# Optimization experiments

Measured on AMD Instinct MI355X. Metric: run time of the kernel, lower is better.

## Reference

```python
import jax, jax.numpy as jnp
import numpy as np

BATCH, DIM, HEADS = 512, 2048, 16
CPH = DIM // HEADS  # per-head channels = 128
EPS = 1e-5


def setup_inputs() -> dict:
    key = jax.random.key(0)
    ks = jax.random.split(key, 6)
    x = jax.random.normal(ks[0], (BATCH, DIM, 1, 1), dtype=jnp.float32)
    W_qv = jax.random.normal(ks[1], (2 * DIM, DIM), dtype=jnp.float32) * (1.0 / np.sqrt(DIM))
    temperature = jnp.ones((HEADS, 1, 1), dtype=jnp.float32)
    k_param = jax.random.normal(ks[2], (BATCH, DIM, 1, 1), dtype=jnp.float32)
    bias_param = jax.random.normal(ks[3], (BATCH, HEADS, CPH * CPH, 1), dtype=jnp.float32)
    bn_gamma = jnp.ones((HEADS,), dtype=jnp.float32)
    bn_beta = jnp.zeros((HEADS,), dtype=jnp.float32)
    W_out = jax.random.normal(ks[4], (DIM, DIM, 1, 1), dtype=jnp.float32) * (1.0 / np.sqrt(DIM))
    b_out = jax.random.normal(ks[5], (DIM,), dtype=jnp.float32) * 0.01
    return {"x": x, "W_qv": W_qv, "temperature": temperature, "k_param": k_param,
            "bias_param": bias_param, "bn_gamma": bn_gamma, "bn_beta": bn_beta,
            "W_out": W_out, "b_out": b_out}


def reference(x, W_qv, temperature, k_param, bias_param, bn_gamma, bn_beta, W_out, b_out):
    b, c, h, w = x.shape  # h = w = 1 (required by x.squeeze() + Linear)
    heads = temperature.shape[0]
    cph = c // heads

    xs = x.reshape(b, c)
    qv = xs @ W_qv.T                     # [b, 2c]
    q, v = qv[:, :c], qv[:, c:]
    q = q.reshape(b, heads, cph, 1)      # b head c (h w)
    v = v.reshape(b, heads, cph, 1)
    k = k_param.reshape(b, heads, cph, 1)

    # BatchNorm2d over channel = head (training-mode batch stats, biased var)
    mean = jnp.mean(v, axis=(0, 2, 3), keepdims=True)
    var = jnp.var(v, axis=(0, 2, 3), keepdims=True)
    v = (v - mean) * jax.lax.rsqrt(var + EPS)
    v = v * bn_gamma.reshape(1, heads, 1, 1) + bn_beta.reshape(1, heads, 1, 1)

    # attn = q @ k^T over the singleton spatial dim -> [b, head, cph, cph]
    attn = jnp.einsum('bhcx,bhdx->bhcd', q, k)
    attn = attn + bias_param.reshape(b, heads, cph, cph)
    attn = attn * temperature  # [heads,1,1] broadcasts over batch
    attn = jax.nn.softmax(attn, axis=-1)

    out = jnp.einsum('bhcd,bhdx->bhcx', attn, v)  # [b, head, cph, 1]
    out = out.reshape(b, c)

    # 1x1 conv == matmul
    out = out @ W_out.reshape(c, c).T + b_out
    return out.reshape(b, c, 1, 1)
```

## Files before the change

### kernel.cpp

```cpp
#include <hip/hip_runtime.h>
#include <hip/hip_bf16.h>
#include <cstdint>

#define NBATCH 512
#define NDIM   2048
#define NHEADS 16
#define NCPH   128

typedef __bf16 bf16x8 __attribute__((ext_vector_type(8)));
typedef __bf16 bf16x4 __attribute__((ext_vector_type(4)));
typedef float  f32x4  __attribute__((ext_vector_type(4)));

__device__ __forceinline__ unsigned short f2bf(float f) {
    uint32_t u = __builtin_bit_cast(uint32_t, f);
    u += 0x7FFFu + ((u >> 16) & 1u);
    return (unsigned short)(u >> 16);
}

__device__ __forceinline__ void gl_lds16(const void* g, void* l) {
    __builtin_amdgcn_global_load_lds(
        (const __attribute__((address_space(1))) void*)g,
        (__attribute__((address_space(3))) void*)l,
        16, 0, 0);
}

__global__ __launch_bounds__(256) void cvt_x(
    const float* __restrict__ x, unsigned short* __restrict__ ox)
{
    const int t = blockIdx.x * 256 + threadIdx.x;
    float4 v = ((const float4*)x)[t];
    ushort4 o;
    o.x = f2bf(v.x); o.y = f2bf(v.y); o.z = f2bf(v.z); o.w = f2bf(v.w);
    ((ushort4*)ox)[t] = o;
}

template<int BN, int BK, bool BNP>
__global__ __launch_bounds__(256) void gemm_tall(
    const unsigned short* __restrict__ Abf, const float* __restrict__ Bf,
    float* __restrict__ C, const float* __restrict__ bias,
    float* __restrict__ bnpart, int M, int N, int K)
{
    constexpr int BM = 128;
    constexpr int MI = 2;
    constexpr int NI = BN / 16;
    constexpr int GA = (BM * BK) / 2048;
    constexpr int BPT4 = (BN * BK) / 1024;
    constexpr int CPRB = BK / 8;

    __shared__ unsigned short As[2][BM * BK];
    __shared__ unsigned short Bs[2][BN * BK];

    const int tid  = threadIdx.x;
    const int lane = tid & 63;
    const int wid  = tid >> 6;
    const int m0   = blockIdx.y * BM;
    const int n0   = blockIdx.x * BN;
    const int fr   = lane & 15;
    const int kq   = lane >> 4;

    f32x4 acc[MI][NI] = {};
    float4 rb[BPT4];

    const int brow = (BPT4 == 2) ? tid / CPRB : tid >> 4;
    const int bch  = (BPT4 == 2) ? tid % CPRB : ((tid & 15) >> 1);
    const int bhalf = (BPT4 == 2) ? 0 : (tid & 1);

    auto loadA = [&](int bs, int k0) {
#pragma unroll
        for (int r = 0; r < GA; r++) {
            const int e    = r * 2048 + tid * 8;
            const int row  = e / BK;
            const int chk  = (e % BK) >> 3;
            gl_lds16(Abf + (size_t)(m0 + row) * K + k0
                         + ((chk ^ (row & 7)) << 3), &As[bs][e]);
        }
    };
    auto loadB = [&](int k0) {
        if constexpr (BPT4 == 2) {
            const float4* g = (const float4*)(Bf + (size_t)(n0 + brow) * K
                                              + k0 + bch * 8);
            rb[0] = g[0];
            rb[1] = g[1];
        } else {
            rb[0] = *(const float4*)(Bf + (size_t)(n0 + brow) * K + k0
                                     + bch * 8 + bhalf * 4);
        }
    };
    auto writeB = [&](int bs) {
        const int base = brow * BK + ((bch ^ (brow & 7)) << 3);
        if constexpr (BPT4 == 2) {
            bf16x8 v;
            v[0] = (__bf16)rb[0].x; v[1] = (__bf16)rb[0].y;
            v[2] = (__bf16)rb[0].z; v[3] = (__bf16)rb[0].w;
            v[4] = (__bf16)rb[1].x; v[5] = (__bf16)rb[1].y;
            v[6] = (__bf16)rb[1].z; v[7] = (__bf16)rb[1].w;
            *(bf16x8*)&Bs[bs][base] = v;
        } else {
            bf16x4 v;
            v[0] = (__bf16)rb[0].x; v[1] = (__bf16)rb[0].y;
            v[2] = (__bf16)rb[0].z; v[3] = (__bf16)rb[0].w;
            *(bf16x4*)&Bs[bs][base + bhalf * 4] = v;
        }
    };
    auto compute = [&](int bs) {
#pragma unroll
        for (int kh = 0; kh < BK / 32; kh++) {
            const int kchunk = kh * 4 + kq;
            bf16x8 af[MI], bfv[NI];
#pragma unroll
            for (int i = 0; i < MI; i++) {
                const int row = wid * 32 + i * 16 + fr;
                af[i] = *(const bf16x8*)&As[bs][row * BK
                        + ((kchunk ^ (row & 7)) << 3)];
            }
#pragma unroll
            for (int j = 0; j < NI; j++) {
                const int row = j * 16 + fr;
                bfv[j] = *(const bf16x8*)&Bs[bs][row * BK
                         + ((kchunk ^ (row & 7)) << 3)];
            }
#pragma unroll
            for (int i = 0; i < MI; i++)
#pragma unroll
                for (int j = 0; j < NI; j++)
                    acc[i][j] = __builtin_amdgcn_mfma_f32_16x16x32_bf16(
                        af[i], bfv[j], acc[i][j], 0, 0, 0);
        }
    };

    loadA(0, 0);
    loadB(0);
    writeB(0);
    __syncthreads();

    const int NT = K / BK;
    int cur = 0;
    for (int t = 0; t < NT - 1; t++) {
        loadB((t + 1) * BK);
        loadA(cur ^ 1, (t + 1) * BK);
        compute(cur);
        writeB(cur ^ 1);
        __syncthreads();
        cur ^= 1;
    }
    compute(cur);

    const int row0 = m0 + wid * 32 + (kq << 2);
    const int col0 = n0 + fr;
#pragma unroll
    for (int j = 0; j < NI; j++) {
        const int cc = col0 + j * 16;
        const float badd = bias ? bias[cc] : 0.0f;
#pragma unroll
        for (int i = 0; i < MI; i++)
#pragma unroll
            for (int r = 0; r < 4; r++)
                C[(size_t)(row0 + i * 16 + r) * N + cc] = acc[i][j][r] + badd;
    }

    if (BNP && n0 >= NDIM) {
        float s = 0.f, ss = 0.f;
#pragma unroll
        for (int i = 0; i < MI; i++)
#pragma unroll
            for (int j = 0; j < NI; j++)
#pragma unroll
                for (int r = 0; r < 4; r++) {
                    const float v = acc[i][j][r];
                    s += v;
                    ss = fmaf(v, v, ss);
                }
#pragma unroll
        for (int off = 32; off; off >>= 1) {
            s  += __shfl_down(s, off);
            ss += __shfl_down(ss, off);
        }
        __shared__ float rs[4], rss[4];
        if (lane == 0) { rs[wid] = s; rss[wid] = ss; }
        __syncthreads();
        if (tid == 0)
            ((float2*)bnpart)[((n0 - NDIM) >> 5) * 4 + (m0 >> 7)] =
                make_float2(rs[0] + rs[1] + rs[2] + rs[3],
                            rss[0] + rss[1] + rss[2] + rss[3]);
    }
}

__global__ __launch_bounds__(256) void attn_k(
    const float* __restrict__ qv, const float* __restrict__ kparam,
    const float* __restrict__ bias, const float* __restrict__ temperature,
    const float* __restrict__ bnpart, const float* __restrict__ gamma,
    const float* __restrict__ beta, unsigned short* __restrict__ aout)
{
    const int bh = blockIdx.x;
    const int b  = bh >> 4;
    const int h  = bh & 15;
    const int tid = threadIdx.x;

    __shared__ float ks[NCPH], vsr[NCPH], s2sh[2];
    if (tid < 32)
        ((float4*)ks)[tid] =
            ((const float4*)(kparam + (size_t)b * NDIM + h * NCPH))[tid];
    else if (tid < 64)
        ((float4*)vsr)[tid - 32] =
            ((const float4*)(qv + (size_t)b * (2 * NDIM) + NDIM + h * NCPH))[tid - 32];

    if (tid < 16) {
        float2 p = ((const float2*)bnpart)[h * 16 + tid];
        float s = p.x, ss = p.y;
#pragma unroll
        for (int off = 8; off; off >>= 1) {
            s  += __shfl_xor(s, off);
            ss += __shfl_xor(ss, off);
        }
        if (tid == 0) {
            const float inv = 1.0f / (NBATCH * NCPH);
            float mean = s * inv;
            float var  = ss * inv - mean * mean;
            float sc   = gamma[h] * rsqrtf(var + 1e-5f);
            s2sh[0] = sc;
            s2sh[1] = beta[h] - mean * sc;
        }
    }

    const int c = tid >> 1, half = tid & 1;
    const float qc   = qv[(size_t)b * (2 * NDIM) + h * NCPH + c];
    const float temp = temperature[h];

    const float4* bp = (const float4*)(bias + ((size_t)bh << 14)
                                       + (size_t)c * NCPH + half * 64);
    float4 l4[16];
#pragma unroll
    for (int j = 0; j < 16; j++) l4[j] = bp[j];

    __syncthreads();
    const float sc = s2sh[0], sh = s2sh[1];
    const float4* kk4 = (const float4*)(ks  + half * 64);
    const float4* vv4 = (const float4*)(vsr + half * 64);

    float s0 = 0.f, s1 = 0.f, o0 = 0.f, o1 = 0.f;
#pragma unroll
    for (int j = 0; j < 16; j++) {
        const float4 bb = l4[j];
        const float4 kx = kk4[j];
        const float4 vx = vv4[j];
        float px = __expf(fmaf(qc, kx.x, bb.x) * temp);
        float py = __expf(fmaf(qc, kx.y, bb.y) * temp);
        float pz = __expf(fmaf(qc, kx.z, bb.z) * temp);
        float pw = __expf(fmaf(qc, kx.w, bb.w) * temp);
        s0 += px; s1 += py; s0 += pz; s1 += pw;
        o0 = fmaf(px, vx.x, o0);
        o1 = fmaf(py, vx.y, o1);
        o0 = fmaf(pz, vx.z, o0);
        o1 = fmaf(pw, vx.w, o1);
    }
    float s = s0 + s1, o = o0 + o1;
    s += __shfl_xor(s, 1);
    o += __shfl_xor(o, 1);

    if (half == 0)
        aout[(size_t)b * NDIM + h * NCPH + c] = f2bf(fmaf(sc, o / s, sh));
}

extern "C" void kernel_launch(void* const* d_in, const int* in_sizes, int n_in,
                              void* d_out, int out_size, void* d_ws, size_t ws_size,
                              hipStream_t stream)
{
    const float* x      = (const float*)d_in[0];
    const float* Wqv    = (const float*)d_in[1];
    const float* temp   = (const float*)d_in[2];
    const float* kparam = (const float*)d_in[3];
    const float* bias   = (const float*)d_in[4];
    const float* gamma  = (const float*)d_in[5];
    const float* beta   = (const float*)d_in[6];
    const float* Wout   = (const float*)d_in[7];
    const float* bout   = (const float*)d_in[8];
    float* out = (float*)d_out;

    char* ws = (char*)d_ws;
    float*          qv     = (float*)(ws);
    unsigned short* ao_bf  = (unsigned short*)(ws + 8388608);
    float*          bnpart = (float*)(ws + 10485760);
    unsigned short* x_bf   = (unsigned short*)(ws + 10487808);

    cvt_x<<<1024, 256, 0, stream>>>(x, x_bf);

    gemm_tall<32, 64, true><<<dim3(128, 4), 256, 0, stream>>>(
        x_bf, Wqv, qv, nullptr, bnpart, NBATCH, 2 * NDIM, NDIM);

    attn_k<<<NBATCH * NHEADS, 256, 0, stream>>>(
        qv, kparam, bias, temp, bnpart, gamma, beta, ao_bf);

    gemm_tall<16, 64, false><<<dim3(128, 4), 256, 0, stream>>>(
        ao_bf, Wout, out, bout, nullptr, NBATCH, NDIM, NDIM);
}
```

Baseline: 184.8 us.

## Keep full-K weight slab resident in LDS and stream A from global registers

Replaces the double-buffered K-tiled GEMM with a kernel that converts a 32-column by full-K slab of the fp32 weights to bf16 once into 128KB of LDS. Each of 8 waves then streams its A rows directly from global memory into registers with a 4-deep software prefetch, with no per-tile barriers. The tile shapes and grids change: the QV GEMM uses BM=256 over 128x2 blocks, and the output GEMM uses BM=128 over 64x4 blocks. The BN partial-stat layout is updated to match. This removes the per-K-step syncs and A staging through LDS, but the large LDS footprint limits occupancy to one block per CU and forces a serial weight-load prologue.

```diff
diff --git a/kernel.cpp b/kernel.cpp
--- a/kernel.cpp
+++ b/kernel.cpp
@@ -8,20 +8,12 @@
 #define NCPH   128
 
 typedef __bf16 bf16x8 __attribute__((ext_vector_type(8)));
-typedef __bf16 bf16x4 __attribute__((ext_vector_type(4)));
 typedef float  f32x4  __attribute__((ext_vector_type(4)));
 
 __device__ __forceinline__ unsigned short f2bf(float f) {
     uint32_t u = __builtin_bit_cast(uint32_t, f);
     u += 0x7FFFu + ((u >> 16) & 1u);
     return (unsigned short)(u >> 16);
-}
-
-__device__ __forceinline__ void gl_lds16(const void* g, void* l) {
-    __builtin_amdgcn_global_load_lds(
-        (const __attribute__((address_space(1))) void*)g,
-        (__attribute__((address_space(3))) void*)l,
-        16, 0, 0);
 }
 
 __global__ __launch_bounds__(256) void cvt_x(
@@ -34,121 +26,77 @@
     ((ushort4*)ox)[t] = o;
 }
 
-template<int BN, int BK, bool BNP>
-__global__ __launch_bounds__(256) void gemm_tall(
+template<int BM, bool BNP>
+__global__ __launch_bounds__(512) void gemm_bres(
     const unsigned short* __restrict__ Abf, const float* __restrict__ Bf,
     float* __restrict__ C, const float* __restrict__ bias,
-    float* __restrict__ bnpart, int M, int N, int K)
-{
-    constexpr int BM = 128;
-    constexpr int MI = 2;
-    constexpr int NI = BN / 16;
-    constexpr int GA = (BM * BK) / 2048;
-    constexpr int BPT4 = (BN * BK) / 1024;
-    constexpr int CPRB = BK / 8;
-
-    __shared__ unsigned short As[2][BM * BK];
-    __shared__ unsigned short Bs[2][BN * BK];
+    float* __restrict__ bnpart, int N)
+{
+    constexpr int MI = BM / 128;
+    __shared__ unsigned short Bs[32 * 2048];
 
     const int tid  = threadIdx.x;
     const int lane = tid & 63;
-    const int wid  = tid >> 6;
+    const int wv   = tid >> 6;
     const int m0   = blockIdx.y * BM;
-    const int n0   = blockIdx.x * BN;
+    const int n0   = blockIdx.x * 32;
     const int fr   = lane & 15;
     const int kq   = lane >> 4;
-
-    f32x4 acc[MI][NI] = {};
-    float4 rb[BPT4];
-
-    const int brow = (BPT4 == 2) ? tid / CPRB : tid >> 4;
-    const int bch  = (BPT4 == 2) ? tid % CPRB : ((tid & 15) >> 1);
-    const int bhalf = (BPT4 == 2) ? 0 : (tid & 1);
-
-    auto loadA = [&](int bs, int k0) {
-#pragma unroll
-        for (int r = 0; r < GA; r++) {
-            const int e    = r * 2048 + tid * 8;
-            const int row  = e / BK;
-            const int chk  = (e % BK) >> 3;
-            gl_lds16(Abf + (size_t)(m0 + row) * K + k0
-                         + ((chk ^ (row & 7)) << 3), &As[bs][e]);
-        }
+    const int mw   = m0 + wv * (MI * 16);
+
+    {
+        const int r  = tid >> 4;
+        const int c0 = tid & 15;
+#pragma unroll
+        for (int it = 0; it < 16; it++) {
+            const int kc = c0 + it * 16;
+            const float4* g = (const float4*)(Bf + (size_t)(n0 + r) * 2048
+                                              + kc * 8);
+            float4 v0 = g[0], v1 = g[1];
+            bf16x8 v;
+            v[0] = (__bf16)v0.x; v[1] = (__bf16)v0.y;
+            v[2] = (__bf16)v0.z; v[3] = (__bf16)v0.w;
+            v[4] = (__bf16)v1.x; v[5] = (__bf16)v1.y;
+            v[6] = (__bf16)v1.z; v[7] = (__bf16)v1.w;
+            *(bf16x8*)&Bs[r * 2048 + ((kc ^ (r & 15)) << 3)] = v;
+        }
+    }
+    __syncthreads();
+
+    f32x4 acc[MI][2] = {};
+    bf16x8 a0[MI], a1[MI], a2[MI], a3[MI];
+
+    auto ldA = [&](bf16x8 (&d)[MI], int t) {
+#pragma unroll
+        for (int i = 0; i < MI; i++)
+            d[i] = *(const bf16x8*)(Abf + (size_t)(mw + i * 16 + fr) * 2048
+                                    + t * 32 + kq * 8);
     };
-    auto loadB = [&](int k0) {
-        if constexpr (BPT4 == 2) {
-            const float4* g = (const float4*)(Bf + (size_t)(n0 + brow) * K
-                                              + k0 + bch * 8);
-            rb[0] = g[0];
-            rb[1] = g[1];
-        } else {
-            rb[0] = *(const float4*)(Bf + (size_t)(n0 + brow) * K + k0
-                                     + bch * 8 + bhalf * 4);
+    auto step = [&](bf16x8 (&a)[MI], int t) {
+#pragma unroll
+        for (int j = 0; j < 2; j++) {
+            const int row = j * 16 + fr;
+            bf16x8 b = *(const bf16x8*)&Bs[row * 2048
+                        + (((4 * t + kq) ^ (row & 15)) << 3)];
+#pragma unroll
+            for (int i = 0; i < MI; i++)
+                acc[i][j] = __builtin_amdgcn_mfma_f32_16x16x32_bf16(
+                    a[i], b, acc[i][j], 0, 0, 0);
         }
     };
-    auto writeB = [&](int bs) {
-        const int base = brow * BK + ((bch ^ (brow & 7)) << 3);
-        if constexpr (BPT4 == 2) {
-            bf16x8 v;
-            v[0] = (__bf16)rb[0].x; v[1] = (__bf16)rb[0].y;
-            v[2] = (__bf16)rb[0].z; v[3] = (__bf16)rb[0].w;
-            v[4] = (__bf16)rb[1].x; v[5] = (__bf16)rb[1].y;
-            v[6] = (__bf16)rb[1].z; v[7] = (__bf16)rb[1].w;
-            *(bf16x8*)&Bs[bs][base] = v;
-        } else {
-            bf16x4 v;
-            v[0] = (__bf16)rb[0].x; v[1] = (__bf16)rb[0].y;
-            v[2] = (__bf16)rb[0].z; v[3] = (__bf16)rb[0].w;
-            *(bf16x4*)&Bs[bs][base + bhalf * 4] = v;
-        }
-    };
-    auto compute = [&](int bs) {
-#pragma unroll
-        for (int kh = 0; kh < BK / 32; kh++) {
-            const int kchunk = kh * 4 + kq;
-            bf16x8 af[MI], bfv[NI];
-#pragma unroll
-            for (int i = 0; i < MI; i++) {
-                const int row = wid * 32 + i * 16 + fr;
-                af[i] = *(const bf16x8*)&As[bs][row * BK
-                        + ((kchunk ^ (row & 7)) << 3)];
-            }
-#pragma unroll
-            for (int j = 0; j < NI; j++) {
-                const int row = j * 16 + fr;
-                bfv[j] = *(const bf16x8*)&Bs[bs][row * BK
-                         + ((kchunk ^ (row & 7)) << 3)];
-            }
-#pragma unroll
-            for (int i = 0; i < MI; i++)
-#pragma unroll
-                for (int j = 0; j < NI; j++)
-                    acc[i][j] = __builtin_amdgcn_mfma_f32_16x16x32_bf16(
-                        af[i], bfv[j], acc[i][j], 0, 0, 0);
-        }
-    };
-
-    loadA(0, 0);
-    loadB(0);
-    writeB(0);
-    __syncthreads();
-
-    const int NT = K / BK;
-    int cur = 0;
-    for (int t = 0; t < NT - 1; t++) {
-        loadB((t + 1) * BK);
-        loadA(cur ^ 1, (t + 1) * BK);
-        compute(cur);
-        writeB(cur ^ 1);
-        __syncthreads();
-        cur ^= 1;
-    }
-    compute(cur);
-
-    const int row0 = m0 + wid * 32 + (kq << 2);
+
+    ldA(a0, 0); ldA(a1, 1); ldA(a2, 2); ldA(a3, 3);
+    for (int t = 0; t < 64; t += 4) {
+        step(a0, t);     if (t + 4 < 64) ldA(a0, t + 4);
+        step(a1, t + 1); if (t + 5 < 64) ldA(a1, t + 5);
+        step(a2, t + 2); if (t + 6 < 64) ldA(a2, t + 6);
+        step(a3, t + 3); if (t + 7 < 64) ldA(a3, t + 7);
+    }
+
+    const int row0 = mw + (kq << 2);
     const int col0 = n0 + fr;
 #pragma unroll
-    for (int j = 0; j < NI; j++) {
+    for (int j = 0; j < 2; j++) {
         const int cc = col0 + j * 16;
         const float badd = bias ? bias[cc] : 0.0f;
 #pragma unroll
@@ -163,7 +111,7 @@
 #pragma unroll
         for (int i = 0; i < MI; i++)
 #pragma unroll
-            for (int j = 0; j < NI; j++)
+            for (int j = 0; j < 2; j++)
 #pragma unroll
                 for (int r = 0; r < 4; r++) {
                     const float v = acc[i][j][r];
@@ -175,13 +123,17 @@
             s  += __shfl_down(s, off);
             ss += __shfl_down(ss, off);
         }
-        __shared__ float rs[4], rss[4];
-        if (lane == 0) { rs[wid] = s; rss[wid] = ss; }
+        float* red = (float*)Bs;
         __syncthreads();
-        if (tid == 0)
-            ((float2*)bnpart)[((n0 - NDIM) >> 5) * 4 + (m0 >> 7)] =
-                make_float2(rs[0] + rs[1] + rs[2] + rs[3],
-                            rss[0] + rss[1] + rss[2] + rss[3]);
+        if (lane == 0) { red[wv] = s; red[8 + wv] = ss; }
+        __syncthreads();
+        if (tid == 0) {
+            float S = 0.f, SS = 0.f;
+#pragma unroll
+            for (int w = 0; w < 8; w++) { S += red[w]; SS += red[8 + w]; }
+            ((float2*)bnpart)[((n0 - NDIM) >> 5) * 2 + (m0 >> 8)] =
+                make_float2(S, SS);
+        }
     }
 }
 
@@ -204,11 +156,11 @@
         ((float4*)vsr)[tid - 32] =
             ((const float4*)(qv + (size_t)b * (2 * NDIM) + NDIM + h * NCPH))[tid - 32];
 
-    if (tid < 16) {
-        float2 p = ((const float2*)bnpart)[h * 16 + tid];
+    if (tid < 8) {
+        float2 p = ((const float2*)bnpart)[h * 8 + tid];
         float s = p.x, ss = p.y;
 #pragma unroll
-        for (int off = 8; off; off >>= 1) {
+        for (int off = 4; off; off >>= 1) {
             s  += __shfl_xor(s, off);
             ss += __shfl_xor(ss, off);
         }
@@ -284,12 +236,12 @@
 
     cvt_x<<<1024, 256, 0, stream>>>(x, x_bf);
 
-    gemm_tall<32, 64, true><<<dim3(128, 4), 256, 0, stream>>>(
-        x_bf, Wqv, qv, nullptr, bnpart, NBATCH, 2 * NDIM, NDIM);
+    gemm_bres<256, true><<<dim3(128, 2), 512, 0, stream>>>(
+        x_bf, Wqv, qv, nullptr, bnpart, 2 * NDIM);
 
     attn_k<<<NBATCH * NHEADS, 256, 0, stream>>>(
         qv, kparam, bias, temp, bnpart, gamma, beta, ao_bf);
 
-    gemm_tall<16, 64, false><<<dim3(128, 4), 256, 0, stream>>>(
-        ao_bf, Wout, out, bout, nullptr, NBATCH, NDIM, NDIM);
-}
+    gemm_bres<128, false><<<dim3(64, 4), 512, 0, stream>>>(
+        ao_bf, Wout, out, bout, nullptr, NDIM);
+}
```

Result: faster. 170.9 us (-7.5%).
